# Performance work log

Measured on AMD Instinct MI355X. Metric: run time of the kernel, lower is better.

Reference implementation:

```python
import jax, jax.numpy as jnp
import numpy as np
import math

B, IN, OUT = 32, 8192, 8192
DENSITY = 0.15

def _inverse_softplus(v):
    return math.log(math.expm1(v))

def setup_inputs() -> dict:
    key = jax.random.key(0)
    k1, k2, k3, k4 = jax.random.split(key, 4)
    inputs = jax.random.normal(k1, (B, IN), dtype=jnp.float32)
    active = jax.random.uniform(k2, (OUT, IN)) < DENSITY
    sign = jnp.where(jax.random.uniform(k3, (OUT, IN)) < 0.5, 1, -1)
    weight_state = jnp.where(active, sign, 0).astype(jnp.int32)
    # log_scale initialized so softplus(log_scale) = 1/sqrt(in_features)
    log_scale = jnp.full((OUT,), _inverse_softplus(1.0 / math.sqrt(IN)), dtype=jnp.float32)
    bias = jax.random.normal(k4, (OUT,), dtype=jnp.float32) * 0.01
    return {"inputs": inputs, "log_scale": log_scale, "bias": bias, "weight_state": weight_state}

def reference(inputs, log_scale, bias, weight_state):
    # scale = softplus(log_scale).clamp_min(1e-4), per output channel
    scale = jnp.maximum(jax.nn.softplus(log_scale), 1e-4)  # [OUT]
    # effective_weight = ternary_state * scale[:, None]; out = x @ W^T + b
    w = weight_state.astype(inputs.dtype) * scale[:, None]  # [OUT, IN]
    return jnp.einsum('bi,oi->bo', inputs, w) + bias
```

## Files before the change

### kernel.cpp

```cpp
#include <hip/hip_runtime.h>
#include <hip/hip_bf16.h>
#include <cmath>

#define B_SZ   32
#define K_SZ   8192
#define N_SZ   8192
#define WAVES  8
#define BLOCK  (WAVES * 64)
#define NTILE  32
#define KCHUNK (K_SZ / WAVES)

typedef __attribute__((ext_vector_type(8))) short bf16x8;
typedef __attribute__((ext_vector_type(4))) float f32x4;

__device__ __forceinline__ unsigned pack_rn(float lo, float hi) {
  unsigned ul = __builtin_bit_cast(unsigned, lo) + 0x8000u;
  unsigned uh = __builtin_bit_cast(unsigned, hi) + 0x8000u;
  return (ul >> 16) | (uh & 0xFFFF0000u);
}

__device__ __forceinline__ unsigned pack_w(int w0, int w1) {
  unsigned u0 = __builtin_bit_cast(unsigned, (float)w0);
  unsigned u1 = __builtin_bit_cast(unsigned, (float)w1);
  return (u0 >> 16) | (u1 & 0xFFFF0000u);
}

__device__ __forceinline__ bf16x8 afrag(float4 a, float4 b) {
  union { unsigned u[4]; bf16x8 v; } t;
  t.u[0] = pack_rn(a.x, a.y);
  t.u[1] = pack_rn(a.z, a.w);
  t.u[2] = pack_rn(b.x, b.y);
  t.u[3] = pack_rn(b.z, b.w);
  return t.v;
}

__device__ __forceinline__ bf16x8 bfrag(int4 a, int4 b) {
  union { unsigned u[4]; bf16x8 v; } t;
  t.u[0] = pack_w(a.x, a.y);
  t.u[1] = pack_w(a.z, a.w);
  t.u[2] = pack_w(b.x, b.y);
  t.u[3] = pack_w(b.z, b.w);
  return t.v;
}

__global__ __launch_bounds__(BLOCK, 2) void ternary_mm(
    const float* __restrict__ X,
    const float* __restrict__ log_scale,
    const float* __restrict__ bias,
    const int*   __restrict__ W,
    float*       __restrict__ out)
{
  __shared__ float red[WAVES][B_SZ][NTILE + 1];

  const int tid  = threadIdx.x;
  const int wv   = tid >> 6;
  const int lane = tid & 63;
  const int q    = lane >> 4;
  const int r    = lane & 15;
  const int nbase = blockIdx.x * NTILE;
  const int kbase = wv * KCHUNK + q * 8;

  const float* xp0 = X + (size_t)r        * K_SZ + kbase;
  const float* xp1 = X + (size_t)(r + 16) * K_SZ + kbase;
  const int* wp0 = W + (size_t)(nbase + r)      * K_SZ + kbase;
  const int* wp1 = W + (size_t)(nbase + 16 + r) * K_SZ + kbase;

  f32x4 acc00 = {0.f,0.f,0.f,0.f}, acc01 = {0.f,0.f,0.f,0.f};
  f32x4 acc10 = {0.f,0.f,0.f,0.f}, acc11 = {0.f,0.f,0.f,0.f};

  #pragma unroll 2
  for (int kb = 0; kb < KCHUNK; kb += 32) {
    float4 a0l = *(const float4*)(xp0 + kb);
    float4 a0h = *(const float4*)(xp0 + kb + 4);
    float4 a1l = *(const float4*)(xp1 + kb);
    float4 a1h = *(const float4*)(xp1 + kb + 4);
    int4   b0l = *(const int4*)(wp0 + kb);
    int4   b0h = *(const int4*)(wp0 + kb + 4);
    int4   b1l = *(const int4*)(wp1 + kb);
    int4   b1h = *(const int4*)(wp1 + kb + 4);

    bf16x8 A0 = afrag(a0l, a0h);
    bf16x8 A1 = afrag(a1l, a1h);
    bf16x8 B0 = bfrag(b0l, b0h);
    bf16x8 B1 = bfrag(b1l, b1h);

    acc00 = __builtin_amdgcn_mfma_f32_16x16x32_bf16(A0, B0, acc00, 0, 0, 0);
    acc01 = __builtin_amdgcn_mfma_f32_16x16x32_bf16(A0, B1, acc01, 0, 0, 0);
    acc10 = __builtin_amdgcn_mfma_f32_16x16x32_bf16(A1, B0, acc10, 0, 0, 0);
    acc11 = __builtin_amdgcn_mfma_f32_16x16x32_bf16(A1, B1, acc11, 0, 0, 0);
  }

  #pragma unroll
  for (int rg = 0; rg < 4; ++rg) {
    red[wv][q * 4 + rg     ][r     ] = acc00[rg];
    red[wv][q * 4 + rg     ][16 + r] = acc01[rg];
    red[wv][16 + q * 4 + rg][r     ] = acc10[rg];
    red[wv][16 + q * 4 + rg][16 + r] = acc11[rg];
  }
  __syncthreads();

  #pragma unroll
  for (int e = 0; e < 2; ++e) {
    int oidx = tid + e * BLOCK;
    int b  = oidx >> 5;
    int nl = oidx & 31;
    float s = 0.f;
    #pragma unroll
    for (int w8 = 0; w8 < WAVES; ++w8) s += red[w8][b][nl];
    int o = nbase + nl;
    float sp    = log1pf(expf(log_scale[o]));
    float scale = fmaxf(sp, 1e-4f);
    out[(size_t)b * N_SZ + o] = s * scale + bias[o];
  }
}

extern "C" void kernel_launch(void* const* d_in, const int* in_sizes, int n_in,
                              void* d_out, int out_size, void* d_ws, size_t ws_size,
                              hipStream_t stream) {
  const float* X  = (const float*)d_in[0];
  const float* ls = (const float*)d_in[1];
  const float* bs = (const float*)d_in[2];
  const int*   W  = (const int*)d_in[3];
  float* out = (float*)d_out;
  ternary_mm<<<N_SZ / NTILE, BLOCK, 0, stream>>>(X, ls, bs, W, out);
}
```

Baseline: 400.1 us.

## Pre-pack X to bf16 fragments, split K across blocks, stage W through LDS

Adds a prep kernel that converts X to bf16 once, laid out in MFMA fragment order in the workspace, so the main kernel no longer reloads and converts fp32 X in every block. The main kernel splits K across two blocks per N-tile and combines the halves with atomicAdd into a zero-initialised output. W tiles are loaded coalesced into LDS with register prefetch, and each wave computes one 16x16 tile. The cost is two extra launches (memset and prep), atomics, and two barriers per K-step, against the main cost of streaming the 256MB int32 weight matrix.

```diff
diff --git a/kernel.cpp b/kernel.cpp
--- a/kernel.cpp
+++ b/kernel.cpp
@@ -2,13 +2,16 @@
 #include <hip/hip_bf16.h>
 #include <cmath>
 
-#define B_SZ   32
+
 #define K_SZ   8192
 #define N_SZ   8192
-#define WAVES  8
-#define BLOCK  (WAVES * 64)
-#define NTILE  32
-#define KCHUNK (K_SZ / WAVES)
+#define B_SZ   32
+#define KSPLIT 2
+#define KHALF  (K_SZ / KSPLIT)
+#define BN     32
+#define BK     128
+#define STEPS  (KHALF / BK)
+#define LDW    132
 
 typedef __attribute__((ext_vector_type(8))) short bf16x8;
 typedef __attribute__((ext_vector_type(4))) float f32x4;
@@ -18,99 +21,113 @@
   unsigned uh = __builtin_bit_cast(unsigned, hi) + 0x8000u;
   return (ul >> 16) | (uh & 0xFFFF0000u);
 }
-
 __device__ __forceinline__ unsigned pack_w(int w0, int w1) {
   unsigned u0 = __builtin_bit_cast(unsigned, (float)w0);
   unsigned u1 = __builtin_bit_cast(unsigned, (float)w1);
   return (u0 >> 16) | (u1 & 0xFFFF0000u);
 }
 
-__device__ __forceinline__ bf16x8 afrag(float4 a, float4 b) {
-  union { unsigned u[4]; bf16x8 v; } t;
-  t.u[0] = pack_rn(a.x, a.y);
-  t.u[1] = pack_rn(a.z, a.w);
-  t.u[2] = pack_rn(b.x, b.y);
-  t.u[3] = pack_rn(b.z, b.w);
-  return t.v;
+__global__ void xprep(const float* __restrict__ X, uint4* __restrict__ Xr) {
+  int t = blockIdx.x * blockDim.x + threadIdx.x;
+  int lane = t & 63;
+  int chunk = t >> 6;
+  int kb = chunk >> 1;
+  int mt = chunk & 1;
+  int row = mt * 16 + (lane & 15);
+  int k0 = kb * 32 + (lane >> 4) * 8;
+  const float* p = X + (size_t)row * K_SZ + k0;
+  float4 a = *(const float4*)p;
+  float4 b = *(const float4*)(p + 4);
+  uint4 o;
+  o.x = pack_rn(a.x, a.y); o.y = pack_rn(a.z, a.w);
+  o.z = pack_rn(b.x, b.y); o.w = pack_rn(b.z, b.w);
+  Xr[t] = o;
 }
 
-__device__ __forceinline__ bf16x8 bfrag(int4 a, int4 b) {
-  union { unsigned u[4]; bf16x8 v; } t;
-  t.u[0] = pack_w(a.x, a.y);
-  t.u[1] = pack_w(a.z, a.w);
-  t.u[2] = pack_w(b.x, b.y);
-  t.u[3] = pack_w(b.z, b.w);
-  return t.v;
-}
-
-__global__ __launch_bounds__(BLOCK, 2) void ternary_mm(
-    const float* __restrict__ X,
+__global__ __launch_bounds__(256, 2) void tmm(
+    const int*   __restrict__ W,
+    const uint4* __restrict__ Xr,
     const float* __restrict__ log_scale,
     const float* __restrict__ bias,
-    const int*   __restrict__ W,
-    float*       __restrict__ out)
-{
-  __shared__ float red[WAVES][B_SZ][NTILE + 1];
+    float*       __restrict__ out) {
+  __shared__ int lds[32 * LDW];
 
   const int tid  = threadIdx.x;
-  const int wv   = tid >> 6;
+  const int w    = tid >> 6;
   const int lane = tid & 63;
   const int q    = lane >> 4;
   const int r    = lane & 15;
-  const int nbase = blockIdx.x * NTILE;
-  const int kbase = wv * KCHUNK + q * 8;
+  const int nb   = blockIdx.x * BN;
+  const int kh   = blockIdx.y;
+  const int mt   = w & 1;
+  const int nt   = w >> 1;
 
-  const float* xp0 = X + (size_t)r        * K_SZ + kbase;
-  const float* xp1 = X + (size_t)(r + 16) * K_SZ + kbase;
-  const int* wp0 = W + (size_t)(nbase + r)      * K_SZ + kbase;
-  const int* wp1 = W + (size_t)(nbase + 16 + r) * K_SZ + kbase;
+  const int srow = 8 * w + (lane >> 5);
+  const int skof = 4 * (lane & 31);
+  const int* gW = W + (size_t)(nb + srow) * K_SZ + (size_t)kh * KHALF + skof;
+  const int lof = srow * LDW + skof;
 
-  f32x4 acc00 = {0.f,0.f,0.f,0.f}, acc01 = {0.f,0.f,0.f,0.f};
-  f32x4 acc10 = {0.f,0.f,0.f,0.f}, acc11 = {0.f,0.f,0.f,0.f};
+  int4 wr0 = *(const int4*)(gW + 0 * 2 * K_SZ);
+  int4 wr1 = *(const int4*)(gW + 1 * 2 * K_SZ);
+  int4 wr2 = *(const int4*)(gW + 2 * 2 * K_SZ);
+  int4 wr3 = *(const int4*)(gW + 3 * 2 * K_SZ);
 
-  #pragma unroll 2
-  for (int kb = 0; kb < KCHUNK; kb += 32) {
-    float4 a0l = *(const float4*)(xp0 + kb);
-    float4 a0h = *(const float4*)(xp0 + kb + 4);
-    float4 a1l = *(const float4*)(xp1 + kb);
-    float4 a1h = *(const float4*)(xp1 + kb + 4);
-    int4   b0l = *(const int4*)(wp0 + kb);
-    int4   b0h = *(const int4*)(wp0 + kb + 4);
-    int4   b1l = *(const int4*)(wp1 + kb);
-    int4   b1h = *(const int4*)(wp1 + kb + 4);
+  const uint4* xr = Xr + lane;
+  const int kbb = kh * (KHALF / 32);
+  uint4 a0 = xr[(size_t)((kbb + 0) * 2 + mt) * 64];
+  uint4 a1 = xr[(size_t)((kbb + 1) * 2 + mt) * 64];
+  uint4 a2 = xr[(size_t)((kbb + 2) * 2 + mt) * 64];
+  uint4 a3 = xr[(size_t)((kbb + 3) * 2 + mt) * 64];
 
-    bf16x8 A0 = afrag(a0l, a0h);
-    bf16x8 A1 = afrag(a1l, a1h);
-    bf16x8 B0 = bfrag(b0l, b0h);
-    bf16x8 B1 = bfrag(b1l, b1h);
+  f32x4 acc = {0.f, 0.f, 0.f, 0.f};
+  const int Rbase = (nt * 16 + r) * LDW;
 
-    acc00 = __builtin_amdgcn_mfma_f32_16x16x32_bf16(A0, B0, acc00, 0, 0, 0);
-    acc01 = __builtin_amdgcn_mfma_f32_16x16x32_bf16(A0, B1, acc01, 0, 0, 0);
-    acc10 = __builtin_amdgcn_mfma_f32_16x16x32_bf16(A1, B0, acc10, 0, 0, 0);
-    acc11 = __builtin_amdgcn_mfma_f32_16x16x32_bf16(A1, B1, acc11, 0, 0, 0);
+  for (int step = 0; step < STEPS; ++step) {
+    __syncthreads();
+    *(int4*)&lds[lof + 0 * 2 * LDW] = wr0;
+    *(int4*)&lds[lof + 1 * 2 * LDW] = wr1;
+    *(int4*)&lds[lof + 2 * 2 * LDW] = wr2;
+    *(int4*)&lds[lof + 3 * 2 * LDW] = wr3;
+    if (step + 1 < STEPS) {
+      const int* g = gW + (step + 1) * BK;
+      wr0 = *(const int4*)(g + 0 * 2 * K_SZ);
+      wr1 = *(const int4*)(g + 1 * 2 * K_SZ);
+      wr2 = *(const int4*)(g + 2 * 2 * K_SZ);
+      wr3 = *(const int4*)(g + 3 * 2 * K_SZ);
+    }
+    __syncthreads();
+
+    uint4 ca0 = a0, ca1 = a1, ca2 = a2, ca3 = a3;
+    if (step + 1 < STEPS) {
+      int kb2 = kbb + (step + 1) * 4;
+      a0 = xr[(size_t)((kb2 + 0) * 2 + mt) * 64];
+      a1 = xr[(size_t)((kb2 + 1) * 2 + mt) * 64];
+      a2 = xr[(size_t)((kb2 + 2) * 2 + mt) * 64];
+      a3 = xr[(size_t)((kb2 + 3) * 2 + mt) * 64];
+    }
+
+    #pragma unroll
+    for (int s = 0; s < 4; ++s) {
+      uint4 ca = (s == 0) ? ca0 : (s == 1) ? ca1 : (s == 2) ? ca2 : ca3;
+      int ro = Rbase + s * 32 + q * 8;
+      int4 b0 = *(const int4*)&lds[ro];
+      int4 b1 = *(const int4*)&lds[ro + 4];
+      union { unsigned u[4]; bf16x8 v; } Bf;
+      Bf.u[0] = pack_w(b0.x, b0.y); Bf.u[1] = pack_w(b0.z, b0.w);
+      Bf.u[2] = pack_w(b1.x, b1.y); Bf.u[3] = pack_w(b1.z, b1.w);
+      bf16x8 Af = __builtin_bit_cast(bf16x8, ca);
+      acc = __builtin_amdgcn_mfma_f32_16x16x32_bf16(Af, Bf.v, acc, 0, 0, 0);
+    }
   }
 
+  const int o = nb + nt * 16 + r;
+  float sp    = log1pf(expf(log_scale[o]));
+  float scale = fmaxf(sp, 1e-4f);
+  float badd  = (kh == 0) ? bias[o] : 0.f;
   #pragma unroll
   for (int rg = 0; rg < 4; ++rg) {
-    red[wv][q * 4 + rg     ][r     ] = acc00[rg];
-    red[wv][q * 4 + rg     ][16 + r] = acc01[rg];
-    red[wv][16 + q * 4 + rg][r     ] = acc10[rg];
-    red[wv][16 + q * 4 + rg][16 + r] = acc11[rg];
-  }
-  __syncthreads();
-
-  #pragma unroll
-  for (int e = 0; e < 2; ++e) {
-    int oidx = tid + e * BLOCK;
-    int b  = oidx >> 5;
-    int nl = oidx & 31;
-    float s = 0.f;
-    #pragma unroll
-    for (int w8 = 0; w8 < WAVES; ++w8) s += red[w8][b][nl];
-    int o = nbase + nl;
-    float sp    = log1pf(expf(log_scale[o]));
-    float scale = fmaxf(sp, 1e-4f);
-    out[(size_t)b * N_SZ + o] = s * scale + bias[o];
+    int b = mt * 16 + q * 4 + rg;
+    atomicAdd(&out[(size_t)b * N_SZ + o], acc[rg] * scale + badd);
   }
 }
 
@@ -122,5 +139,10 @@
   const float* bs = (const float*)d_in[2];
   const int*   W  = (const int*)d_in[3];
   float* out = (float*)d_out;
-  ternary_mm<<<N_SZ / NTILE, BLOCK, 0, stream>>>(X, ls, bs, W, out);
+  uint4* Xr = (uint4*)d_ws;
+
+  hipMemsetAsync(out, 0, (size_t)B_SZ * N_SZ * sizeof(float), stream);
+  xprep<<<128, 256, 0, stream>>>(X, Xr);
+  dim3 grid(N_SZ / BN, KSPLIT);
+  tmm<<<grid, 256, 0, stream>>>(W, Xr, ls, bs, out);
 }
```

New measurement: 366.3 us. 1.09x faster.
